# Performance work log

Hardware: AMD Instinct MI355X
Metric: run time of the kernel (lower is better)

The kernel has to match this reference:

```python
import jax, jax.numpy as jnp
import numpy as np

FEATURE_DIM = 512
SQRT_DIM = float(np.sqrt(FEATURE_DIM))


def setup_inputs() -> dict:
    key = jax.random.key(0)
    x = jax.random.normal(key, (5, FEATURE_DIM, 128, 256), dtype=jnp.float32)
    return {"x": x, "record_len": 4}


def reference(x, record_len):
    # x: [max_cav, C, H, W]; record_len: python int (number of valid CAVs)
    max_cav, C, H, W = x.shape
    # tokens: [H*W, max_cav, C]
    tokens = x.reshape(max_cav, C, H * W).transpose(2, 0, 1)
    # scores: [H*W, max_cav, max_cav]
    score = jnp.einsum('bqc,bkc->bqk', tokens, tokens) / SQRT_DIM
    # pad mask over key dim: keys with index >= record_len are invalid
    pad_mask = jnp.arange(max_cav) >= record_len            # [max_cav]
    score = jnp.where(pad_mask[None, None, :], -jnp.inf, score)
    attn = jax.nn.softmax(score, axis=-1)
    attn = jnp.nan_to_num(attn, nan=0.0)                    # all-masked rows -> 0
    context = jnp.einsum('bqk,bkc->bqc', attn, tokens)      # [H*W, max_cav, C]
    ego = context[:, 0, :]                                  # [H*W, C]
    return ego.T.reshape(C, H, W)[None]                     # [1, C, H, W]
```

## Files before the change

kernel.cpp:

```cpp
#include <hip/hip_runtime.h>
#include <math.h>

#define KMAX   5
#define NC     512
#define HW     32768
#define NCHUNK 32
#define CPC    (NC / NCHUNK)
#define INV_SQRT_DIM 0.044194173824159216f

__device__ __forceinline__ int clamp_K(const int* __restrict__ rlp) {
    int K = *rlp;
    return K < 0 ? 0 : (K > KMAX ? KMAX : K);
}

template <int K>
__device__ __forceinline__ void k1_dots_body(const float4* __restrict__ xv,
                                             float4* __restrict__ pv,
                                             int b4, int chunk) {
    float4 d[K];
#pragma unroll
    for (int k = 0; k < K; ++k) d[k] = make_float4(0.f, 0.f, 0.f, 0.f);

    const int c0 = chunk * CPC;
#pragma unroll 4
    for (int i = 0; i < CPC; ++i) {
        const int c = c0 + i;
        const float4 x0 = xv[(size_t)c * (HW / 4) + b4];
        d[0].x += x0.x * x0.x; d[0].y += x0.y * x0.y;
        d[0].z += x0.z * x0.z; d[0].w += x0.w * x0.w;
#pragma unroll
        for (int k = 1; k < K; ++k) {
            const float4 xk = xv[((size_t)k * NC + c) * (HW / 4) + b4];
            d[k].x += x0.x * xk.x; d[k].y += x0.y * xk.y;
            d[k].z += x0.z * xk.z; d[k].w += x0.w * xk.w;
        }
    }
#pragma unroll
    for (int k = 0; k < K; ++k)
        pv[((size_t)chunk * KMAX + k) * (HW / 4) + b4] = d[k];
}

__global__ void k1_partial_dots(const float* __restrict__ x,
                                const int* __restrict__ rlp,
                                float* __restrict__ partial) {
    const int b4    = blockIdx.x * blockDim.x + threadIdx.x;
    const int chunk = blockIdx.y;
    const int K     = clamp_K(rlp);
    const float4* xv = (const float4*)x;
    float4*       pv = (float4*)partial;
    switch (K) {
        case 1: k1_dots_body<1>(xv, pv, b4, chunk); break;
        case 2: k1_dots_body<2>(xv, pv, b4, chunk); break;
        case 3: k1_dots_body<3>(xv, pv, b4, chunk); break;
        case 4: k1_dots_body<4>(xv, pv, b4, chunk); break;
        case 5: k1_dots_body<5>(xv, pv, b4, chunk); break;
        default: break;
    }
}

template <int K>
__device__ __forceinline__ void k2_body(const float* __restrict__ partial,
                                        float* __restrict__ attn, int b) {
    float d[K];
#pragma unroll
    for (int k = 0; k < K; ++k) d[k] = 0.f;
#pragma unroll 4
    for (int ch = 0; ch < NCHUNK; ++ch) {
#pragma unroll
        for (int k = 0; k < K; ++k)
            d[k] += partial[((size_t)ch * KMAX + k) * HW + b];
    }
    float m = -INFINITY;
#pragma unroll
    for (int k = 0; k < K; ++k) { d[k] *= INV_SQRT_DIM; m = fmaxf(m, d[k]); }
    float s = 0.f;
#pragma unroll
    for (int k = 0; k < K; ++k) { d[k] = expf(d[k] - m); s += d[k]; }
    const float inv = 1.f / s;
#pragma unroll
    for (int k = 0; k < KMAX; ++k)
        attn[(size_t)k * HW + b] = (k < K) ? d[k] * inv : 0.f;
}

__global__ void k2_softmax(const float* __restrict__ partial,
                           const int* __restrict__ rlp,
                           float* __restrict__ attn) {
    const int b = blockIdx.x * blockDim.x + threadIdx.x;
    const int K = clamp_K(rlp);
    switch (K) {
        case 1: k2_body<1>(partial, attn, b); break;
        case 2: k2_body<2>(partial, attn, b); break;
        case 3: k2_body<3>(partial, attn, b); break;
        case 4: k2_body<4>(partial, attn, b); break;
        case 5: k2_body<5>(partial, attn, b); break;
        default:
#pragma unroll
            for (int k = 0; k < KMAX; ++k) attn[(size_t)k * HW + b] = 0.f;
            break;
    }
}

template <int K>
__device__ __forceinline__ void k3_body(const float4* __restrict__ xv,
                                        const float4* __restrict__ av,
                                        float4* __restrict__ outv,
                                        int b4, int c) {
    float4 acc = make_float4(0.f, 0.f, 0.f, 0.f);
#pragma unroll
    for (int k = 0; k < K; ++k) {
        const float4 a  = av[(size_t)k * (HW / 4) + b4];
        const float4 xk = xv[((size_t)k * NC + c) * (HW / 4) + b4];
        acc.x += a.x * xk.x; acc.y += a.y * xk.y;
        acc.z += a.z * xk.z; acc.w += a.w * xk.w;
    }
    outv[(size_t)c * (HW / 4) + b4] = acc;
}

__global__ void k3_out(const float* __restrict__ x,
                       const int* __restrict__ rlp,
                       const float* __restrict__ attn,
                       float* __restrict__ out) {
    const int idx = blockIdx.x * blockDim.x + threadIdx.x;
    const int b4  = idx & (HW / 4 - 1);
    const int c   = idx >> 13;
    const int K   = clamp_K(rlp);
    const float4* xv   = (const float4*)x;
    const float4* av   = (const float4*)attn;
    float4*       outv = (float4*)out;
    switch (K) {
        case 1: k3_body<1>(xv, av, outv, b4, c); break;
        case 2: k3_body<2>(xv, av, outv, b4, c); break;
        case 3: k3_body<3>(xv, av, outv, b4, c); break;
        case 4: k3_body<4>(xv, av, outv, b4, c); break;
        case 5: k3_body<5>(xv, av, outv, b4, c); break;
        default:
            outv[(size_t)c * (HW / 4) + b4] = make_float4(0.f, 0.f, 0.f, 0.f);
            break;
    }
}

__global__ void k1_full_softmax(const float* __restrict__ x,
                                const int* __restrict__ rlp,
                                float* __restrict__ attn) {
    const int b4 = blockIdx.x * blockDim.x + threadIdx.x;
    const int K  = clamp_K(rlp);
    const float4* xv = (const float4*)x;

    float4 d[KMAX];
#pragma unroll
    for (int k = 0; k < KMAX; ++k) d[k] = make_float4(0.f, 0.f, 0.f, 0.f);

#pragma unroll 4
    for (int c = 0; c < NC; ++c) {
        const float4 x0 = xv[(size_t)c * (HW / 4) + b4];
        d[0].x += x0.x * x0.x; d[0].y += x0.y * x0.y;
        d[0].z += x0.z * x0.z; d[0].w += x0.w * x0.w;
#pragma unroll
        for (int k = 1; k < KMAX; ++k) {
            if (k < K) {
                const float4 xk = xv[((size_t)k * NC + c) * (HW / 4) + b4];
                d[k].x += x0.x * xk.x; d[k].y += x0.y * xk.y;
                d[k].z += x0.z * xk.z; d[k].w += x0.w * xk.w;
            }
        }
    }

    float4 m = make_float4(-INFINITY, -INFINITY, -INFINITY, -INFINITY);
#pragma unroll
    for (int k = 0; k < KMAX; ++k)
        if (k < K) {
            d[k].x *= INV_SQRT_DIM; d[k].y *= INV_SQRT_DIM;
            d[k].z *= INV_SQRT_DIM; d[k].w *= INV_SQRT_DIM;
            m.x = fmaxf(m.x, d[k].x); m.y = fmaxf(m.y, d[k].y);
            m.z = fmaxf(m.z, d[k].z); m.w = fmaxf(m.w, d[k].w);
        }
    float4 s = make_float4(0.f, 0.f, 0.f, 0.f);
#pragma unroll
    for (int k = 0; k < KMAX; ++k)
        if (k < K) {
            d[k].x = expf(d[k].x - m.x); d[k].y = expf(d[k].y - m.y);
            d[k].z = expf(d[k].z - m.z); d[k].w = expf(d[k].w - m.w);
            s.x += d[k].x; s.y += d[k].y; s.z += d[k].z; s.w += d[k].w;
        }
    float4 inv = make_float4(0.f, 0.f, 0.f, 0.f);
    if (K > 0) { inv.x = 1.f / s.x; inv.y = 1.f / s.y; inv.z = 1.f / s.z; inv.w = 1.f / s.w; }

    float4* av = (float4*)attn;
#pragma unroll
    for (int k = 0; k < KMAX; ++k) {
        float4 a = make_float4(0.f, 0.f, 0.f, 0.f);
        if (k < K) {
            a.x = d[k].x * inv.x; a.y = d[k].y * inv.y;
            a.z = d[k].z * inv.z; a.w = d[k].w * inv.w;
        }
        av[(size_t)k * (HW / 4) + b4] = a;
    }
}

extern "C" void kernel_launch(void* const* d_in, const int* in_sizes, int n_in,
                              void* d_out, int out_size, void* d_ws, size_t ws_size,
                              hipStream_t stream) {
    const float* x   = (const float*)d_in[0];
    const int*   rl  = (const int*)d_in[1];
    float*       out = (float*)d_out;
    float*       ws  = (float*)d_ws;

    const size_t partial_elems = (size_t)NCHUNK * KMAX * HW;
    const size_t attn_elems    = (size_t)KMAX * HW;

    if (ws_size >= (partial_elems + attn_elems) * sizeof(float)) {
        float* partial = ws;
        float* attn    = ws + partial_elems;
        k1_partial_dots<<<dim3((HW / 4) / 256, NCHUNK), 256, 0, stream>>>(x, rl, partial);
        k2_softmax<<<HW / 256, 256, 0, stream>>>(partial, rl, attn);
        k3_out<<<(NC * (HW / 4)) / 256, 256, 0, stream>>>(x, rl, attn, out);
    } else {
        float* attn = ws;
        k1_full_softmax<<<(HW / 4) / 256, 256, 0, stream>>>(x, rl, attn);
        k3_out<<<(NC * (HW / 4)) / 256, 256, 0, stream>>>(x, rl, attn, out);
    }
}
```

Before: 493.8 us.

## Coarsen dot and output kernels per thread and use nontemporal memory ops

The partial-dot kernel now has each thread handle two float4 columns, which halves the grid in x. The output kernel has each thread loop over 8 channels and reuse the attention weights it loaded once, instead of reloading them for every channel. Nontemporal loads and stores are added for the streamed x reads, the partial reads and the output writes, so these one-touch streams pollute the cache less. Fewer threads may reduce memory-level parallelism on a kernel that is bandwidth bound.

```diff
diff --git a/kernel.cpp b/kernel.cpp
--- a/kernel.cpp
+++ b/kernel.cpp
@@ -4,9 +4,13 @@
 #define KMAX   5
 #define NC     512
 #define HW     32768
+#define HW4    (HW / 4)
 #define NCHUNK 32
 #define CPC    (NC / NCHUNK)
+#define CG     8
 #define INV_SQRT_DIM 0.044194173824159216f
+
+typedef float vfloat4 __attribute__((ext_vector_type(4)));
 
 __device__ __forceinline__ int clamp_K(const int* __restrict__ rlp) {
     int K = *rlp;
@@ -14,46 +18,48 @@
 }
 
 template <int K>
-__device__ __forceinline__ void k1_dots_body(const float4* __restrict__ xv,
-                                             float4* __restrict__ pv,
-                                             int b4, int chunk) {
-    float4 d[K];
-#pragma unroll
-    for (int k = 0; k < K; ++k) d[k] = make_float4(0.f, 0.f, 0.f, 0.f);
+__device__ __forceinline__ void k1_body(const vfloat4* __restrict__ xv,
+                                        vfloat4* __restrict__ pv,
+                                        int b4, int chunk) {
+    vfloat4 da[K], db[K];
+#pragma unroll
+    for (int k = 0; k < K; ++k) { da[k] = (vfloat4)0.f; db[k] = (vfloat4)0.f; }
 
     const int c0 = chunk * CPC;
-#pragma unroll 4
+#pragma unroll 2
     for (int i = 0; i < CPC; ++i) {
         const int c = c0 + i;
-        const float4 x0 = xv[(size_t)c * (HW / 4) + b4];
-        d[0].x += x0.x * x0.x; d[0].y += x0.y * x0.y;
-        d[0].z += x0.z * x0.z; d[0].w += x0.w * x0.w;
+        const vfloat4 x0a = xv[(size_t)c * HW4 + b4];
+        const vfloat4 x0b = xv[(size_t)c * HW4 + b4 + 256];
+        da[0] += x0a * x0a;  db[0] += x0b * x0b;
 #pragma unroll
         for (int k = 1; k < K; ++k) {
-            const float4 xk = xv[((size_t)k * NC + c) * (HW / 4) + b4];
-            d[k].x += x0.x * xk.x; d[k].y += x0.y * xk.y;
-            d[k].z += x0.z * xk.z; d[k].w += x0.w * xk.w;
-        }
-    }
-#pragma unroll
-    for (int k = 0; k < K; ++k)
-        pv[((size_t)chunk * KMAX + k) * (HW / 4) + b4] = d[k];
+            const vfloat4 xka = xv[((size_t)k * NC + c) * HW4 + b4];
+            const vfloat4 xkb = xv[((size_t)k * NC + c) * HW4 + b4 + 256];
+            da[k] += x0a * xka;  db[k] += x0b * xkb;
+        }
+    }
+#pragma unroll
+    for (int k = 0; k < K; ++k) {
+        pv[((size_t)chunk * KMAX + k) * HW4 + b4]       = da[k];
+        pv[((size_t)chunk * KMAX + k) * HW4 + b4 + 256] = db[k];
+    }
 }
 
 __global__ void k1_partial_dots(const float* __restrict__ x,
                                 const int* __restrict__ rlp,
                                 float* __restrict__ partial) {
-    const int b4    = blockIdx.x * blockDim.x + threadIdx.x;
+    const int b4    = blockIdx.x * 512 + threadIdx.x;
     const int chunk = blockIdx.y;
     const int K     = clamp_K(rlp);
-    const float4* xv = (const float4*)x;
-    float4*       pv = (float4*)partial;
+    const vfloat4* xv = (const vfloat4*)x;
+    vfloat4*       pv = (vfloat4*)partial;
     switch (K) {
-        case 1: k1_dots_body<1>(xv, pv, b4, chunk); break;
-        case 2: k1_dots_body<2>(xv, pv, b4, chunk); break;
-        case 3: k1_dots_body<3>(xv, pv, b4, chunk); break;
-        case 4: k1_dots_body<4>(xv, pv, b4, chunk); break;
-        case 5: k1_dots_body<5>(xv, pv, b4, chunk); break;
+        case 1: k1_body<1>(xv, pv, b4, chunk); break;
+        case 2: k1_body<2>(xv, pv, b4, chunk); break;
+        case 3: k1_body<3>(xv, pv, b4, chunk); break;
+        case 4: k1_body<4>(xv, pv, b4, chunk); break;
+        case 5: k1_body<5>(xv, pv, b4, chunk); break;
         default: break;
     }
 }
@@ -64,11 +70,11 @@
     float d[K];
 #pragma unroll
     for (int k = 0; k < K; ++k) d[k] = 0.f;
-#pragma unroll 4
+#pragma unroll
     for (int ch = 0; ch < NCHUNK; ++ch) {
 #pragma unroll
         for (int k = 0; k < K; ++k)
-            d[k] += partial[((size_t)ch * KMAX + k) * HW + b];
+            d[k] += __builtin_nontemporal_load(&partial[((size_t)ch * KMAX + k) * HW + b]);
     }
     float m = -INFINITY;
 #pragma unroll
@@ -101,40 +107,49 @@
 }
 
 template <int K>
-__device__ __forceinline__ void k3_body(const float4* __restrict__ xv,
-                                        const float4* __restrict__ av,
-                                        float4* __restrict__ outv,
-                                        int b4, int c) {
-    float4 acc = make_float4(0.f, 0.f, 0.f, 0.f);
-#pragma unroll
-    for (int k = 0; k < K; ++k) {
-        const float4 a  = av[(size_t)k * (HW / 4) + b4];
-        const float4 xk = xv[((size_t)k * NC + c) * (HW / 4) + b4];
-        acc.x += a.x * xk.x; acc.y += a.y * xk.y;
-        acc.z += a.z * xk.z; acc.w += a.w * xk.w;
-    }
-    outv[(size_t)c * (HW / 4) + b4] = acc;
+__device__ __forceinline__ void k3_body(const vfloat4* __restrict__ xv,
+                                        const vfloat4* __restrict__ av,
+                                        vfloat4* __restrict__ outv,
+                                        int b4, int c0) {
+    vfloat4 a[K];
+#pragma unroll
+    for (int k = 0; k < K; ++k) a[k] = av[(size_t)k * HW4 + b4];
+
+#pragma unroll 4
+    for (int j = 0; j < CG; ++j) {
+        const int c = c0 + j;
+        vfloat4 acc = (vfloat4)0.f;
+#pragma unroll
+        for (int k = 0; k < K; ++k) {
+            const vfloat4 xk =
+                __builtin_nontemporal_load(&xv[((size_t)k * NC + c) * HW4 + b4]);
+            acc += a[k] * xk;
+        }
+        __builtin_nontemporal_store(acc, &outv[(size_t)c * HW4 + b4]);
+    }
 }
 
 __global__ void k3_out(const float* __restrict__ x,
                        const int* __restrict__ rlp,
                        const float* __restrict__ attn,
                        float* __restrict__ out) {
-    const int idx = blockIdx.x * blockDim.x + threadIdx.x;
-    const int b4  = idx & (HW / 4 - 1);
-    const int c   = idx >> 13;
-    const int K   = clamp_K(rlp);
-    const float4* xv   = (const float4*)x;
-    const float4* av   = (const float4*)attn;
-    float4*       outv = (float4*)out;
+    const int b4 = blockIdx.x * blockDim.x + threadIdx.x;
+    const int c0 = blockIdx.y * CG;
+    const int K  = clamp_K(rlp);
+    const vfloat4* xv   = (const vfloat4*)x;
+    const vfloat4* av   = (const vfloat4*)attn;
+    vfloat4*       outv = (vfloat4*)out;
     switch (K) {
-        case 1: k3_body<1>(xv, av, outv, b4, c); break;
-        case 2: k3_body<2>(xv, av, outv, b4, c); break;
-        case 3: k3_body<3>(xv, av, outv, b4, c); break;
-        case 4: k3_body<4>(xv, av, outv, b4, c); break;
-        case 5: k3_body<5>(xv, av, outv, b4, c); break;
+        case 1: k3_body<1>(xv, av, outv, b4, c0); break;
+        case 2: k3_body<2>(xv, av, outv, b4, c0); break;
+        case 3: k3_body<3>(xv, av, outv, b4, c0); break;
+        case 4: k3_body<4>(xv, av, outv, b4, c0); break;
+        case 5: k3_body<5>(xv, av, outv, b4, c0); break;
         default:
-            outv[(size_t)c * (HW / 4) + b4] = make_float4(0.f, 0.f, 0.f, 0.f);
+#pragma unroll
+            for (int j = 0; j < CG; ++j)
+                __builtin_nontemporal_store((vfloat4)0.f,
+                                            &outv[(size_t)(c0 + j) * HW4 + b4]);
             break;
     }
 }
@@ -144,57 +159,48 @@
                                 float* __restrict__ attn) {
     const int b4 = blockIdx.x * blockDim.x + threadIdx.x;
     const int K  = clamp_K(rlp);
-    const float4* xv = (const float4*)x;
-
-    float4 d[KMAX];
-#pragma unroll
-    for (int k = 0; k < KMAX; ++k) d[k] = make_float4(0.f, 0.f, 0.f, 0.f);
+    const vfloat4* xv = (const vfloat4*)x;
+
+    vfloat4 d[KMAX];
+#pragma unroll
+    for (int k = 0; k < KMAX; ++k) d[k] = (vfloat4)0.f;
 
 #pragma unroll 4
     for (int c = 0; c < NC; ++c) {
-        const float4 x0 = xv[(size_t)c * (HW / 4) + b4];
-        d[0].x += x0.x * x0.x; d[0].y += x0.y * x0.y;
-        d[0].z += x0.z * x0.z; d[0].w += x0.w * x0.w;
+        const vfloat4 x0 = xv[(size_t)c * HW4 + b4];
+        d[0] += x0 * x0;
 #pragma unroll
         for (int k = 1; k < KMAX; ++k) {
             if (k < K) {
-                const float4 xk = xv[((size_t)k * NC + c) * (HW / 4) + b4];
-                d[k].x += x0.x * xk.x; d[k].y += x0.y * xk.y;
-                d[k].z += x0.z * xk.z; d[k].w += x0.w * xk.w;
+                const vfloat4 xk = xv[((size_t)k * NC + c) * HW4 + b4];
+                d[k] += x0 * xk;
             }
         }
     }
 
-    float4 m = make_float4(-INFINITY, -INFINITY, -INFINITY, -INFINITY);
+    vfloat4 m = (vfloat4)(-INFINITY);
 #pragma unroll
     for (int k = 0; k < KMAX; ++k)
         if (k < K) {
-            d[k].x *= INV_SQRT_DIM; d[k].y *= INV_SQRT_DIM;
-            d[k].z *= INV_SQRT_DIM; d[k].w *= INV_SQRT_DIM;
+            d[k] *= INV_SQRT_DIM;
             m.x = fmaxf(m.x, d[k].x); m.y = fmaxf(m.y, d[k].y);
             m.z = fmaxf(m.z, d[k].z); m.w = fmaxf(m.w, d[k].w);
         }
-    float4 s = make_float4(0.f, 0.f, 0.f, 0.f);
+    vfloat4 s = (vfloat4)0.f;
 #pragma unroll
     for (int k = 0; k < KMAX; ++k)
         if (k < K) {
             d[k].x = expf(d[k].x - m.x); d[k].y = expf(d[k].y - m.y);
             d[k].z = expf(d[k].z - m.z); d[k].w = expf(d[k].w - m.w);
-            s.x += d[k].x; s.y += d[k].y; s.z += d[k].z; s.w += d[k].w;
-        }
-    float4 inv = make_float4(0.f, 0.f, 0.f, 0.f);
+            s += d[k];
+        }
+    vfloat4 inv = (vfloat4)0.f;
     if (K > 0) { inv.x = 1.f / s.x; inv.y = 1.f / s.y; inv.z = 1.f / s.z; inv.w = 1.f / s.w; }
 
-    float4* av = (float4*)attn;
-#pragma unroll
-    for (int k = 0; k < KMAX; ++k) {
-        float4 a = make_float4(0.f, 0.f, 0.f, 0.f);
-        if (k < K) {
-            a.x = d[k].x * inv.x; a.y = d[k].y * inv.y;
-            a.z = d[k].z * inv.z; a.w = d[k].w * inv.w;
-        }
-        av[(size_t)k * (HW / 4) + b4] = a;
-    }
+    vfloat4* av = (vfloat4*)attn;
+#pragma unroll
+    for (int k = 0; k < KMAX; ++k)
+        av[(size_t)k * HW4 + b4] = (k < K) ? d[k] * inv : (vfloat4)0.f;
 }
 
 extern "C" void kernel_launch(void* const* d_in, const int* in_sizes, int n_in,
@@ -211,12 +217,12 @@
     if (ws_size >= (partial_elems + attn_elems) * sizeof(float)) {
         float* partial = ws;
         float* attn    = ws + partial_elems;
-        k1_partial_dots<<<dim3((HW / 4) / 256, NCHUNK), 256, 0, stream>>>(x, rl, partial);
+        k1_partial_dots<<<dim3(HW4 / 512, NCHUNK), 256, 0, stream>>>(x, rl, partial);
         k2_softmax<<<HW / 256, 256, 0, stream>>>(partial, rl, attn);
-        k3_out<<<(NC * (HW / 4)) / 256, 256, 0, stream>>>(x, rl, attn, out);
+        k3_out<<<dim3(HW4 / 256, NC / CG), 256, 0, stream>>>(x, rl, attn, out);
     } else {
         float* attn = ws;
-        k1_full_softmax<<<(HW / 4) / 256, 256, 0, stream>>>(x, rl, attn);
-        k3_out<<<(NC * (HW / 4)) / 256, 256, 0, stream>>>(x, rl, attn, out);
-    }
-}
+        k1_full_softmax<<<HW4 / 256, 256, 0, stream>>>(x, rl, attn);
+        k3_out<<<dim3(HW4 / 256, NC / CG), 256, 0, stream>>>(x, rl, attn, out);
+    }
+}
```

Result: slower. 512.8 us (+3.8%).
